# Optimization experiments

Hardware: AMD Instinct MI355X
Metric: run time of the kernel (lower is better)

The kernel has to match this reference:

```python
import jax, jax.numpy as jnp
import numpy as np

B, A, C, L, NH, SCALE = 1, 5, 64, 4, 8, 2
H = W = 24
S = 2 * C
KS = 5


def layernorm(x, g, b, eps=1e-5):
    m = x.mean(-1, keepdims=True)
    v = ((x - m) ** 2).mean(-1, keepdims=True)
    return (x - m) * jax.lax.rsqrt(v + eps) * g + b


def pe_1d(n, d):
    # PositionEncoding: temperature**(2*(i//2)/d), sin of even cols then cos of odd cols
    g = jnp.arange(d, dtype=jnp.float32)
    g = 10000.0 ** (2.0 * jnp.floor(g / 2.0) / d)
    p = jnp.arange(n, dtype=jnp.float32)[:, None] / g[None, :]
    return jnp.concatenate([jnp.sin(p[:, 0::2]), jnp.cos(p[:, 1::2])], axis=1)  # [n, d]


def mha(qk, v, in_w, out_w, nh, mask=None):
    # qk, v: [Lq, Bt, D]; torch nn.MultiheadAttention, bias-free, q=k=qk, value=v
    Lq, Bt, D = qk.shape
    dh = D // nh
    wq, wk, wv = jnp.split(in_w, 3, axis=0)
    q = (qk @ wq.T).reshape(Lq, Bt, nh, dh)
    k = (qk @ wk.T).reshape(Lq, Bt, nh, dh)
    vv = (v @ wv.T).reshape(Lq, Bt, nh, dh)
    s = jnp.einsum('lbhd,mbhd->bhlm', q, k) / jnp.sqrt(jnp.float32(dh))
    if mask is not None:
        s = s + mask
    a = jax.nn.softmax(s, axis=-1)
    o = jnp.einsum('bhlm,mbhd->lbhd', a, vv).reshape(Lq, Bt, D)
    return o @ out_w.T


def unfold3x3(x):
    # F.unfold(k=3, pad=1).permute(2,0,1): [N,c,h,w] -> [h*w, N, 9c] (c, kh, kw ordering)
    N, c, h, w = x.shape
    xp = jnp.pad(x, ((0, 0), (0, 0), (1, 1), (1, 1)))
    p = jnp.stack([xp[:, :, i:i + h, j:j + w] for i in range(3) for j in range(3)], axis=2)
    return p.reshape(N, c * 9, h * w).transpose(2, 0, 1)


def conv_hw(x5, w):
    # Conv3d kernel (1,3,3) pad (0,1,1): 2D conv per angular view
    Bc, Ci, Aa, h, w_ = x5.shape
    y = jax.lax.conv_general_dilated(
        x5.transpose(0, 2, 1, 3, 4).reshape(Bc * Aa, Ci, h, w_), w, (1, 1), ((1, 1), (1, 1)),
        dimension_numbers=('NCHW', 'OIHW', 'NCHW'))
    return y.reshape(Bc, Aa, w.shape[0], h, w_).transpose(0, 2, 1, 3, 4)


def window_mask(h, w, k):
    # SpaTrans.gen_mask: additive -inf outside a k x k local window
    kl, kr = k // 2, k - k // 2
    i = jnp.arange(h)
    j = jnp.arange(w)
    mh = (i[None, :] >= i[:, None] - kl) & (i[None, :] < i[:, None] + kr)
    mw = (j[None, :] >= j[:, None] - kl) & (j[None, :] < j[:, None] + kr)
    m = (mh[:, None, :, None] & mw[None, :, None, :]).reshape(h * w, h * w)
    return jnp.where(m, 0.0, -jnp.inf).astype(jnp.float32)


def setup_inputs() -> dict:
    key = jax.random.key(0)
    ks = iter(jax.random.split(key, 64))
    def nrm(shape, s=0.02):
        return jax.random.normal(next(ks), shape, dtype=jnp.float32) * s
    d = {}
    d['lr'] = jax.random.normal(next(ks), (B, 1, A * H, A * W), dtype=jnp.float32)
    Hh, Wh = H * SCALE, W * SCALE
    ch = -1.0 + (2.0 * jnp.arange(Hh, dtype=jnp.float32) + 1.0) / Hh
    cw = -1.0 + (2.0 * jnp.arange(Wh, dtype=jnp.float32) + 1.0) / Wh
    g = jnp.stack(jnp.meshgrid(ch, cw, indexing='ij'), axis=-1).reshape(-1, 2)
    d['coord'] = jnp.broadcast_to(g, (B, Hh * Wh, 2))
    d['conv0_w'] = nrm((C, 1, 3, 3), 0.1)
    d['convi_w'] = nrm((3, C, C, 3, 3), 0.05)
    d['ang_ln_g'] = jnp.ones((L, C)); d['ang_ln_b'] = jnp.zeros((L, C))
    d['ang_in'] = nrm((L, 3 * C, C)); d['ang_out'] = nrm((L, C, C))
    d['ang_ff_g'] = jnp.ones((L, C)); d['ang_ff_b'] = jnp.zeros((L, C))
    d['ang_w1'] = nrm((L, 2 * C, C)); d['ang_w2'] = nrm((L, C, 2 * C))
    d['spa_mlp'] = nrm((L, S, 9 * C))
    d['spa_ln_g'] = jnp.ones((L, S)); d['spa_ln_b'] = jnp.zeros((L, S))
    d['spa_in'] = nrm((L, 3 * S, S)); d['spa_out'] = nrm((L, S, S))
    d['spa_ff_g'] = jnp.ones((L, S)); d['spa_ff_b'] = jnp.zeros((L, S))
    d['spa_w1'] = nrm((L, 2 * S, S)); d['spa_w2'] = nrm((L, S, 2 * S))
    d['spa_lin'] = nrm((L, C, S))
    IN = A * A * C + 2 + 2 * A * A
    d['imp_w0'] = nrm((320, IN)); d['imp_b0'] = jnp.zeros((320,))
    d['imp_w1'] = nrm((320, 320)); d['imp_b1'] = jnp.zeros((320,))
    d['imp_w2'] = nrm((3 * A * A, 320)); d['imp_b2'] = jnp.zeros((3 * A * A,))
    return d


def reference(lr, coord, conv0_w, convi_w, ang_ln_g, ang_ln_b, ang_in, ang_out,
              ang_ff_g, ang_ff_b, ang_w1, ang_w2, spa_mlp, spa_ln_g, spa_ln_b,
              spa_in, spa_out, spa_ff_g, spa_ff_b, spa_w1, spa_w2, spa_lin,
              imp_w0, imp_b0, imp_w1, imp_b1, imp_w2, imp_b2):
    Bn = lr.shape[0]
    # 'b c (a1 h) (a2 w) -> b c (a1 a2) h w'
    x = lr.reshape(Bn, 1, A, H, A, W).transpose(0, 1, 2, 4, 3, 5).reshape(Bn, 1, A * A, H, W)
    spa_pe_img = ((pe_1d(H, C)[:, None, :] + pe_1d(W, C)[None, :, :]) * 0.5).transpose(2, 0, 1)[None]  # [1,C,h,w]
    ang_pe = pe_1d(A * A, C)[:, None, :]  # [A^2,1,C]
    buf = conv_hw(x, conv0_w)
    t = buf
    for i in range(3):
        t = jax.nn.leaky_relu(conv_hw(t, convi_w[i]), 0.2)
    buf = t + buf
    mask = window_mask(H, W, KS)
    blk = buf
    for l in range(L):
        # ---- AngTrans: tokens [A^2, B*h*w, C]
        tok = blk.transpose(2, 0, 3, 4, 1).reshape(A * A, Bn * H * W, C)
        tn = layernorm(tok + ang_pe, ang_ln_g[l], ang_ln_b[l])
        tok = mha(tn, tok, ang_in[l], ang_out[l], NH) + tok
        ff = layernorm(tok, ang_ff_g[l], ang_ff_b[l])
        tok = jax.nn.relu(ff @ ang_w1[l].T) @ ang_w2[l].T + tok
        blk = tok.reshape(A * A, Bn, H, W, C).transpose(1, 4, 0, 2, 3)
        # ---- SpaTrans: tokens [h*w, B*A^2, 2C] with local-window mask
        xb = blk.transpose(0, 2, 1, 3, 4).reshape(Bn * A * A, C, H, W)
        tok = unfold3x3(xb) @ spa_mlp[l].T
        pe_tok = unfold3x3(spa_pe_img) @ spa_mlp[l].T
        tn = layernorm(tok + pe_tok, spa_ln_g[l], spa_ln_b[l])
        tok = mha(tn, tok, spa_in[l], spa_out[l], NH, mask) + tok
        ff = layernorm(tok, spa_ff_g[l], spa_ff_b[l])
        tok = jax.nn.relu(ff @ spa_w1[l].T) @ spa_w2[l].T + tok
        t5 = tok.reshape(H, W, Bn, A * A, S).transpose(2, 4, 3, 0, 1)  # b s a h w
        blk = jnp.einsum('os,bsahw->boahw', spa_lin[l], t5)  # 1x1x1 Conv3d
    buf = blk + buf
    # 'b c (a1 a2) h w -> b c (a1 h) (a2 w)'
    feat_lr = buf.reshape(Bn, C, A, A, H, W).transpose(0, 1, 2, 4, 3, 5).reshape(Bn, C, A * H, A * W)
    Hh, Wh = H * SCALE, W * SCALE
    # per-view bilinear upsample (align_corners=False)
    v = feat_lr.reshape(Bn, C, A, H, A, W).transpose(0, 2, 4, 1, 3, 5).reshape(Bn * A * A, C, H, W)
    v = jax.image.resize(v, (Bn * A * A, C, Hh, Wh), method='bilinear')
    feat_hr = v.reshape(Bn, A, A, C, Hh, Wh).transpose(0, 4, 5, 1, 2, 3).reshape(Bn, Hh, Wh, A * A * C)
    # nearest grid_sample of LR cell-center coords -> relative coord
    c_ = jnp.clip(coord + 1e-6, -1 + 1e-6, 1 - 1e-6)
    ih = jnp.clip(jnp.round(((c_[..., 0] + 1) * H - 1) / 2), 0, H - 1)
    iw = jnp.clip(jnp.round(((c_[..., 1] + 1) * W - 1) / 2), 0, W - 1)
    qh = -1.0 + (2.0 * ih + 1.0) / H
    qw = -1.0 + (2.0 * iw + 1.0) / W
    rel = jnp.stack([(coord[..., 0] - qh) * H, (coord[..., 1] - qw) * W], axis=-1).reshape(Bn, Hh, Wh, 2)
    au = 0.5 + jnp.arange(A, dtype=jnp.float32)  # make_coord ranges [0,A]
    ca = jnp.stack(jnp.meshgrid(au, au, indexing='ij'), axis=-1).reshape(-1)
    ca = jnp.broadcast_to(ca, (Bn, Hh, Wh, 2 * A * A))
    inp = jnp.concatenate([feat_hr, rel, ca], axis=-1)
    h0 = jax.nn.relu(inp @ imp_w0.T + imp_b0)
    h1 = jax.nn.relu(h0 @ imp_w1.T + imp_b1)
    o = h1 @ imp_w2.T + imp_b2
    # 'b h w (a1 a2 c) -> b c (a1 h) (a2 w)', c=3
    return o.reshape(Bn, Hh, Wh, A, A, 3).transpose(0, 5, 3, 1, 4, 2).reshape(Bn, 3, A * Hh, A * Wh)
```

## Files before the change

kernel.cpp:

```cpp
#include <hip/hip_runtime.h>
#include <math.h>

typedef short  s16x4 __attribute__((ext_vector_type(4)));
typedef short  s16x8 __attribute__((ext_vector_type(8)));
typedef float  f32x4 __attribute__((ext_vector_type(4)));

static const size_t PE25_  = 0;
static const size_t SPAPE_ = 2048;
static const size_t X_     = 38912;
static const size_t CAV_   = 53312;
static const size_t PETOK_ = 54272;
static const size_t W9C_   = 349184;
static const size_t W9S_   = 459776;
static const size_t BUF_   = 754688;
static const size_t BLK_   = 1676288;
static const size_t ATOK_  = 2597888;
static const size_t TNF_   = 3519488;
static const size_t STOK_  = 4441088;
static const size_t STOK2_ = 6284288;
static const size_t QKV_   = 9970688;
static const size_t WS_FLOATS = 15500288;
static const size_t T0_ = QKV_ + 2764800;
static const size_t T1_ = T0_ + 921600;
static const size_t ZP_ = QKV_;
static const size_t H0_ = STOK_;
static const size_t H1_ = STOK2_;

__device__ inline ushort f2bf(float x) {
  unsigned u = __float_as_uint(x);
  u += 0x7fffu + ((u >> 16) & 1u);
  return (ushort)(u >> 16);
}
__device__ inline float bf2f(ushort h) { return __uint_as_float(((unsigned)h) << 16); }

__device__ inline void store_split(char* p, f32x4 v) {
  s16x4 hi, lo;
  #pragma unroll
  for (int e = 0; e < 4; ++e) {
    float x = v[e];
    ushort h = f2bf(x);
    ushort l = f2bf(x - bf2f(h));
    hi[e] = (short)h; lo[e] = (short)l;
  }
  *(s16x4*)p = hi;
  *(s16x4*)(p + 1024) = lo;
}

__device__ inline void scatter_split(char* base, int rr, int c6, float v) {
  ushort hi = f2bf(v);
  ushort lo = f2bf(v - bf2f(hi));
  int ks = c6 >> 5, kh = (c6 >> 4) & 1, k4 = (c6 >> 2) & 3;
  int lane2 = (k4 >> 1)*32 + ((rr & 15) << 1) + (k4 & 1);
  int byt = (((rr >> 4)*2 + ks) << 11) + (kh << 9) + (lane2 << 3) + (c6 & 3)*2;
  *(ushort*)(base + byt) = hi;
  *(ushort*)(base + byt + 1024) = lo;
}

__device__ inline void ld_bf16x16(const ushort* p, float* dst) {
  s16x8 a = *(const s16x8*)p;
  s16x8 b = *(const s16x8*)(p + 8);
  #pragma unroll
  for (int e = 0; e < 8; ++e) { dst[e] = bf2f((ushort)a[e]); dst[8 + e] = bf2f((ushort)b[e]); }
}

__device__ inline void slot_decode(int i, int wave, int lane,
                                   int& row, int& kof, int& wo) {
  int idx = (i << 2) + wave;
  int msub = idx >> 2, ks = (idx >> 1) & 1, kh = idx & 1;
  int rsub = (lane >> 1) & 15;
  int ksub = ((lane >> 5) << 3) + ((lane & 1) << 2);
  row = (msub << 4) + rsub;
  kof = (ks << 5) + (kh << 4) + ksub;
  wo = ((msub * 2 + ks) << 11) + (kh << 9) + (lane << 3);
}

__device__ inline void mfma_step(const char* ldsA, const char* ldsB, int lane,
                                 int wr, int wc, f32x4 acc[2][2]) {
  #pragma unroll
  for (int ks = 0; ks < 2; ++ks) {
    s16x8 ah[2], al[2], bh[2], bl[2];
    #pragma unroll
    for (int i = 0; i < 2; ++i) {
      const char* pa = ldsA + (((wr*2 + i)*2 + ks) << 11) + (lane << 4);
      ah[i] = *(const s16x8*)pa;
      al[i] = *(const s16x8*)(pa + 1024);
      const char* pb = ldsB + (((wc*2 + i)*2 + ks) << 11) + (lane << 4);
      bh[i] = *(const s16x8*)pb;
      bl[i] = *(const s16x8*)(pb + 1024);
    }
    #pragma unroll
    for (int i = 0; i < 2; ++i) {
      #pragma unroll
      for (int j = 0; j < 2; ++j) {
        acc[i][j] = __builtin_amdgcn_mfma_f32_16x16x32_bf16(ah[i], bh[j], acc[i][j], 0, 0, 0);
        acc[i][j] = __builtin_amdgcn_mfma_f32_16x16x32_bf16(ah[i], bl[j], acc[i][j], 0, 0, 0);
        acc[i][j] = __builtin_amdgcn_mfma_f32_16x16x32_bf16(al[i], bh[j], acc[i][j], 0, 0, 0);
      }
    }
  }
}

__device__ inline void epilogue(f32x4 acc[2][2], const float* bias, const float* res,
                                float* out, int N, int m0, int n0,
                                int wr, int wc, int lane, int act) {
  int colb = n0 + wc*32 + (lane & 15);
  int rowb = m0 + wr*32 + ((lane >> 4) << 2);
  #pragma unroll
  for (int j = 0; j < 2; ++j) {
    int cc = colb + j*16;
    if (cc >= N) continue;
    float bv = bias ? bias[cc] : 0.f;
    #pragma unroll
    for (int i = 0; i < 2; ++i) {
      #pragma unroll
      for (int r = 0; r < 4; ++r) {
        int rr = rowb + i*16 + r;
        float v = acc[i][j][r] + bv;
        if (act == 1) v = fmaxf(v, 0.f);
        else if (act == 2) v = v > 0.f ? v : 0.2f*v;
        if (res) v += res[(long)rr*N + cc];
        if (act == 3) {
          int hh = rr / 48, ww2 = rr % 48, q = cc / 3, ch = cc % 3;
          out[ch*57600 + ((q/5)*48 + hh)*240 + (q%5)*48 + ww2] = v;
        } else if (act == 4) {
          ((ushort*)out)[(long)rr*N + cc] = f2bf(v);
        } else {
          out[(long)rr*N + cc] = v;
        }
      }
    }
  }
}

template<int K>
__global__ __launch_bounds__(256) void qkvg_k(
    const float* __restrict__ A, const float* __restrict__ pe, int pe_mode,
    const float* __restrict__ g, const float* __restrict__ bb,
    const float* __restrict__ W, float* __restrict__ out,
    int NTr0, int NTr1, int N, int Mreal, int Mpad) {
  constexpr int NCH = K / 64;
  __shared__ char Apl[NCH * 16384];
  __shared__ char Bp[16384];
  __shared__ float sw_[4][64][2];
  __shared__ float sf_[64][2];
  int bid = blockIdx.x;
  int type = bid / Mpad, m = bid % Mpad;
  if (m >= Mreal) return;
  int m0 = m*64;
  int NTr = type ? NTr1 : NTr0;
  int ntbase = type ? NTr0 : 0;
  int t = threadIdx.x, lane = t & 63, wave = t >> 6;
  int wr = wave >> 1, wc = wave & 1;

  if (type == 0) {
    f32x4 rv[NCH][4];
    float sA[4], sQ[4];
    #pragma unroll
    for (int i = 0; i < 4; ++i) { sA[i] = 0.f; sQ[i] = 0.f; }
    #pragma unroll
    for (int ch = 0; ch < NCH; ++ch)
      #pragma unroll
      for (int i = 0; i < 4; ++i) {
        int row, kof, wo;
        slot_decode(i, wave, lane, row, kof, wo);
        int gk = ch*64 + kof;
        f32x4 av = *(const f32x4*)&A[(long)(m0 + row)*K + gk];
        if (pe_mode == 0)      av += *(const f32x4*)&pe[(long)(m0/576)*K + gk];
        else                   av += *(const f32x4*)&pe[(long)(m0%576 + row)*K + gk];
        rv[ch][i] = av;
        #pragma unroll
        for (int e = 0; e < 4; ++e) { sA[i] += av[e]; sQ[i] = fmaf(av[e], av[e], sQ[i]); }
      }
    #pragma unroll
    for (int i = 0; i < 4; ++i) {
      float s = sA[i], q = sQ[i];
      s += __shfl_xor(s, 1, 64);  q += __shfl_xor(q, 1, 64);
      s += __shfl_xor(s, 32, 64); q += __shfl_xor(q, 32, 64);
      if ((lane & 1) == 0 && lane < 32) {
        int row = i*16 + (lane >> 1);
        sw_[wave][row][0] = s; sw_[wave][row][1] = q;
      }
    }
    __syncthreads();
    if (t < 64) {
      float s = sw_[0][t][0] + sw_[1][t][0] + sw_[2][t][0] + sw_[3][t][0];
      float q = sw_[0][t][1] + sw_[1][t][1] + sw_[2][t][1] + sw_[3][t][1];
      float mean = s / K, var = q / K - mean*mean;
      sf_[t][0] = mean; sf_[t][1] = rsqrtf(var + 1e-5f);
    }
    __syncthreads();
    #pragma unroll
    for (int ch = 0; ch < NCH; ++ch)
      #pragma unroll
      for (int i = 0; i < 4; ++i) {
        int row, kof, wo;
        slot_decode(i, wave, lane, row, kof, wo);
        int gk = ch*64 + kof;
        float mean = sf_[row][0], rstd = sf_[row][1];
        f32x4 gv = *(const f32x4*)&g[gk];
        f32x4 bv = *(const f32x4*)&bb[gk];
        f32x4 nv;
        #pragma unroll
        for (int e = 0; e < 4; ++e) nv[e] = (rv[ch][i][e] - mean)*rstd*gv[e] + bv[e];
        store_split(Apl + ch*16384 + wo, nv);
      }
  } else {
    #pragma unroll
    for (int ch = 0; ch < NCH; ++ch)
      #pragma unroll
      for (int i = 0; i < 4; ++i) {
        int row, kof, wo;
        slot_decode(i, wave, lane, row, kof, wo);
        f32x4 av = *(const f32x4*)&A[(long)(m0 + row)*K + ch*64 + kof];
        store_split(Apl + ch*16384 + wo, av);
      }
  }

  int S = NTr * NCH;
  f32x4 pb[4];
  #pragma unroll
  for (int i = 0; i < 4; ++i) {
    int row, kof, wo;
    slot_decode(i, wave, lane, row, kof, wo);
    pb[i] = *(const f32x4*)&W[(long)(ntbase*64 + row)*K + kof];
  }
  f32x4 acc[2][2];
  #pragma unroll
  for (int i = 0; i < 2; ++i)
    #pragma unroll
    for (int j = 0; j < 2; ++j) acc[i][j] = (f32x4){0.f,0.f,0.f,0.f};
  for (int s = 0; s < S; ++s) {
    int nt = s / NCH, ch = s % NCH;
    __syncthreads();
    #pragma unroll
    for (int i = 0; i < 4; ++i) {
      int row, kof, wo;
      slot_decode(i, wave, lane, row, kof, wo);
      store_split(Bp + wo, pb[i]);
    }
    __syncthreads();
    if (s + 1 < S) {
      int ntn = (s+1) / NCH, chn = (s+1) % NCH;
      #pragma unroll
      for (int i = 0; i < 4; ++i) {
        int row, kof, wo;
        slot_decode(i, wave, lane, row, kof, wo);
        pb[i] = *(const f32x4*)&W[(long)((ntbase+ntn)*64 + row)*K + chn*64 + kof];
      }
    }
    mfma_step(Apl + ch*16384, Bp, lane, wr, wc, acc);
    if (ch == NCH - 1) {
      epilogue(acc, nullptr, nullptr, out, N, m0, (ntbase+nt)*64, wr, wc, lane, 4);
      #pragma unroll
      for (int i = 0; i < 2; ++i)
        #pragma unroll
        for (int j = 0; j < 2; ++j) acc[i][j] = (f32x4){0.f,0.f,0.f,0.f};
    }
  }
}

template<int K, int LN>
__global__ __launch_bounds__(256) void mgemm3_k(
    const float* __restrict__ A, const float* __restrict__ A2, int nsplit,
    const float* __restrict__ pe, int pe_mode,
    const float* __restrict__ g, const float* __restrict__ bb,
    const float* __restrict__ W, const float* __restrict__ bias,
    const float* __restrict__ res, float* __restrict__ out,
    int N, int act, int Mreal, int Mpad) {
  constexpr int NCH = K / 64;
  __shared__ char Apl[NCH * 16384];
  __shared__ char Bp[16384];
  int bid = blockIdx.x;
  int m = bid % Mpad, nt = bid / Mpad;
  if (m >= Mreal) return;
  int m0 = m*64, n0 = nt*64;
  int t = threadIdx.x, lane = t & 63, wave = t >> 6;
  int wr = wave >> 1, wc = wave & 1;
  const float* As = LN ? A2 : A;
  #pragma unroll
  for (int ch = 0; ch < NCH; ++ch)
    #pragma unroll
    for (int i = 0; i < 4; ++i) {
      int row, kof, wo;
      slot_decode(i, wave, lane, row, kof, wo);
      f32x4 av = *(const f32x4*)&As[(long)(m0 + row)*K + ch*64 + kof];
      store_split(Apl + ch*16384 + wo, av);
    }
  f32x4 pb[4];
  #pragma unroll
  for (int i = 0; i < 4; ++i) {
    int row, kof, wo;
    slot_decode(i, wave, lane, row, kof, wo);
    int br = n0 + row;
    pb[i] = (br < N) ? *(const f32x4*)&W[(long)br*K + kof] : (f32x4){0.f,0.f,0.f,0.f};
  }
  __syncthreads();
  f32x4 acc[2][2];
  #pragma unroll
  for (int i = 0; i < 2; ++i)
    #pragma unroll
    for (int j = 0; j < 2; ++j) acc[i][j] = (f32x4){0.f,0.f,0.f,0.f};
  for (int ch = 0; ch < NCH; ++ch) {
    #pragma unroll
    for (int i = 0; i < 4; ++i) {
      int row, kof, wo;
      slot_decode(i, wave, lane, row, kof, wo);
      store_split(Bp + wo, pb[i]);
    }
    __syncthreads();
    if (ch + 1 < NCH) {
      #pragma unroll
      for (int i = 0; i < 4; ++i) {
        int row, kof, wo;
        slot_decode(i, wave, lane, row, kof, wo);
        int br = n0 + row;
        pb[i] = (br < N) ? *(const f32x4*)&W[(long)br*K + (ch+1)*64 + kof]
                         : (f32x4){0.f,0.f,0.f,0.f};
      }
    }
    mfma_step(Apl + ch*16384, Bp, lane, wr, wc, acc);
    if (ch + 1 < NCH) __syncthreads();
  }
  epilogue(acc, bias, res, out, N, m0, n0, wr, wc, lane, act);
}

__global__ __launch_bounds__(256) void cgemm3_k(
    const float* __restrict__ in, const float* __restrict__ W9, long wstride,
    const float* __restrict__ res, float* __restrict__ out, long ostride,
    int N, int act, int Mreal, int Mpad) {
  __shared__ float halo[144 * 68];
  __shared__ char Ap[16384], Bp[16384];
  int bid = blockIdx.x;
  int m = bid % Mpad, nt = bid / Mpad;
  if (m >= Mreal) return;
  int ly = blockIdx.y;
  W9  += (long)ly * wstride;
  out += (long)ly * ostride;
  int m0 = m*64, n0 = nt*64;
  int a = m0 / 576, off = m0 % 576;
  int h_lo = off/24 - 1, h_hi = (off + 63)/24 + 1;
  int RH = h_hi - h_lo + 1;
  int t = threadIdx.x, lane = t & 63, wave = t >> 6;
  int wr = wave >> 1, wc = wave & 1;
  for (int sidx = t; sidx < RH*24*16; sidx += 256) {
    int tokr = sidx >> 4, c4 = (sidx & 15) << 2;
    int h = h_lo + tokr/24, w = tokr % 24;
    f32x4 v = {0.f,0.f,0.f,0.f};
    if ((unsigned)h < 24u) v = *(const f32x4*)&in[(long)(a*576 + h*24 + w)*64 + c4];
    *(f32x4*)&halo[tokr*68 + c4] = v;
  }
  f32x4 pb[4];
  #pragma unroll
  for (int i = 0; i < 4; ++i) {
    int row, kof, wo;
    slot_decode(i, wave, lane, row, kof, wo);
    int br = n0 + row;
    pb[i] = (br < N) ? *(const f32x4*)&W9[(long)br*64 + kof] : (f32x4){0.f,0.f,0.f,0.f};
  }
  __syncthreads();
  f32x4 acc[2][2];
  #pragma unroll
  for (int i = 0; i < 2; ++i)
    #pragma unroll
    for (int j = 0; j < 2; ++j) acc[i][j] = (f32x4){0.f,0.f,0.f,0.f};
  for (int ij = 0; ij < 9; ++ij) {
    int di = ij/3 - 1, dj = ij%3 - 1;
    #pragma unroll
    for (int i = 0; i < 4; ++i) {
      int row, kof, wo;
      slot_decode(i, wave, lane, row, kof, wo);
      int tok = off + row;
      int h2 = tok/24 + di, w2 = tok%24 + dj;
      f32x4 v = {0.f,0.f,0.f,0.f};
      if ((unsigned)h2 < 24u && (unsigned)w2 < 24u)
        v = *(const f32x4*)&halo[((h2 - h_lo)*24 + w2)*68 + kof];
      store_split(Ap + wo, v);
      store_split(Bp + wo, pb[i]);
    }
    __syncthreads();
    if (ij < 8) {
      #pragma unroll
      for (int i = 0; i < 4; ++i) {
        int row, kof, wo;
        slot_decode(i, wave, lane, row, kof, wo);
        int br = n0 + row;
        pb[i] = (br < N) ? *(const f32x4*)&W9[((long)(ij+1)*N + br)*64 + kof]
                         : (f32x4){0.f,0.f,0.f,0.f};
      }
    }
    mfma_step(Ap, Bp, lane, wr, wc, acc);
    if (ij < 8) __syncthreads();
  }
  epilogue(acc, nullptr, res, out, N, m0, n0, wr, wc, lane, act);
}

__global__ __launch_bounds__(256) void ang_mega_k(
    const ushort* __restrict__ qkv, const float* __restrict__ Wout,
    const float* __restrict__ blkr, const float* __restrict__ g,
    const float* __restrict__ bb, float* __restrict__ atok, float* __restrict__ tnf) {
  int hw = blockIdx.x;
  __shared__ float lq[25*192];
  __shared__ float lao[25*64];
  __shared__ float po[25*68];
  __shared__ float wout[64*65];
  __shared__ float st[25][2];
  int t = threadIdx.x;
  for (int idx = t; idx < 600; idx += 256) {
    int a3 = idx / 24, c8 = (idx % 24) * 8;
    s16x8 r = *(const s16x8*)&qkv[(long)(a3*576 + hw)*192 + c8];
    #pragma unroll
    for (int e = 0; e < 8; ++e) lq[a3*192 + c8 + e] = bf2f((ushort)r[e]);
  }
  for (int idx = t; idx < 4096; idx += 256) {
    int c = idx >> 6, d = idx & 63;
    wout[c*65 + d] = Wout[idx];
  }
  __syncthreads();
  if (t < 200) {
    int l = t / 8, head = t & 7;
    const float* q = lq + l*192 + head*8;
    float s[25]; float mx = -1e30f;
    #pragma unroll
    for (int mm = 0; mm < 25; ++mm) {
      const float* kk = lq + mm*192 + 64 + head*8;
      float acc = 0.f;
      #pragma unroll
      for (int d = 0; d < 8; ++d) acc = fmaf(q[d], kk[d], acc);
      acc *= 0.3535533905932738f;
      s[mm] = acc; mx = fmaxf(mx, acc);
    }
    float sum = 0.f;
    #pragma unroll
    for (int mm = 0; mm < 25; ++mm) { s[mm] = expf(s[mm] - mx); sum += s[mm]; }
    float inv = 1.f / sum;
    #pragma unroll
    for (int d = 0; d < 8; ++d) {
      float acc = 0.f;
      #pragma unroll
      for (int mm = 0; mm < 25; ++mm) acc = fmaf(s[mm], lq[mm*192 + 128 + head*8 + d], acc);
      lao[l*64 + head*8 + d] = acc * inv;
    }
  }
  __syncthreads();
  for (int idx = t; idx < 1600; idx += 256) {
    int tok = idx >> 6, c = idx & 63;
    const float* ar = &lao[tok*64];
    const float* wr = &wout[c*65];
    float accp = 0.f;
    #pragma unroll 16
    for (int d = 0; d < 64; ++d) accp = fmaf(ar[d], wr[d], accp);
    po[tok*68 + c] = accp + blkr[(long)(tok*576 + hw)*64 + c];
  }
  __syncthreads();
  if (t < 25) {
    float s = 0.f, q = 0.f;
    for (int c = 0; c < 64; ++c) { float x = po[t*68 + c]; s += x; q = fmaf(x, x, q); }
    float mean = s / 64.f, var = q / 64.f - mean*mean;
    st[t][0] = mean; st[t][1] = rsqrtf(var + 1e-5f);
  }
  __syncthreads();
  for (int idx = t; idx < 1600; idx += 256) {
    int tok = idx >> 6, c = idx & 63;
    float x = po[tok*68 + c];
    long gidx = (long)(tok*576 + hw)*64 + c;
    atok[gidx] = x;
    tnf[gidx] = (x - st[tok][0]) * st[tok][1] * g[c] + bb[c];
  }
}

__global__ __launch_bounds__(256) void ffn_ang_k(
    const float* __restrict__ tnf, const float* __restrict__ w1,
    const float* __restrict__ w2, float* __restrict__ atok,
    int Mreal, int Mpad) {
  __shared__ char Ap[16384], Bp[16384], Hp[2][16384];
  int bid = blockIdx.x;
  int m = bid % Mpad;
  if (m >= Mreal) return;
  int m0 = m*64;
  int t = threadIdx.x, lane = t & 63, wave = t >> 6;
  int wr = wave >> 1, wc = wave & 1;
  #pragma unroll
  for (int i = 0; i < 4; ++i) {
    int row, kof, wo;
    slot_decode(i, wave, lane, row, kof, wo);
    f32x4 av = *(const f32x4*)&tnf[(long)(m0 + row)*64 + kof];
    store_split(Ap + wo, av);
  }
  f32x4 pb[4];
  #pragma unroll
  for (int i = 0; i < 4; ++i) {
    int row, kof, wo;
    slot_decode(i, wave, lane, row, kof, wo);
    pb[i] = *(const f32x4*)&w1[(long)row*64 + kof];
  }
  __syncthreads();
  for (int nt = 0; nt < 2; ++nt) {
    #pragma unroll
    for (int i = 0; i < 4; ++i) {
      int row, kof, wo;
      slot_decode(i, wave, lane, row, kof, wo);
      store_split(Bp + wo, pb[i]);
    }
    __syncthreads();
    #pragma unroll
    for (int i = 0; i < 4; ++i) {
      int row, kof, wo;
      slot_decode(i, wave, lane, row, kof, wo);
      pb[i] = (nt == 0) ? *(const f32x4*)&w1[(long)(64 + row)*64 + kof]
                        : *(const f32x4*)&w2[(long)row*128 + kof];
    }
    f32x4 acc[2][2];
    #pragma unroll
    for (int i = 0; i < 2; ++i)
      #pragma unroll
      for (int j = 0; j < 2; ++j) acc[i][j] = (f32x4){0.f,0.f,0.f,0.f};
    mfma_step(Ap, Bp, lane, wr, wc, acc);
    #pragma unroll
    for (int jj = 0; jj < 2; ++jj)
      #pragma unroll
      for (int ii = 0; ii < 2; ++ii)
        #pragma unroll
        for (int r = 0; r < 4; ++r) {
          int rr = wr*32 + ii*16 + ((lane >> 4) << 2) + r;
          int cc = wc*32 + jj*16 + (lane & 15);
          scatter_split(Hp[nt], rr, cc, fmaxf(acc[ii][jj][r], 0.f));
        }
    __syncthreads();
  }
  f32x4 acc2[2][2];
  #pragma unroll
  for (int i = 0; i < 2; ++i)
    #pragma unroll
    for (int j = 0; j < 2; ++j) acc2[i][j] = (f32x4){0.f,0.f,0.f,0.f};
  for (int ch = 0; ch < 2; ++ch) {
    #pragma unroll
    for (int i = 0; i < 4; ++i) {
      int row, kof, wo;
      slot_decode(i, wave, lane, row, kof, wo);
      store_split(Bp + wo, pb[i]);
    }
    __syncthreads();
    if (ch == 0) {
      #pragma unroll
      for (int i = 0; i < 4; ++i) {
        int row, kof, wo;
        slot_decode(i, wave, lane, row, kof, wo);
        pb[i] = *(const f32x4*)&w2[(long)row*128 + 64 + kof];
      }
    }
    mfma_step(Hp[ch], Bp, lane, wr, wc, acc2);
    if (ch == 0) __syncthreads();
  }
  epilogue(acc2, nullptr, atok, atok, 64, m0, 0, wr, wc, lane, 0);
}

__global__ __launch_bounds__(512) void megaspa_k(
    const ushort* __restrict__ qkv, const float* __restrict__ stok,
    const float* __restrict__ wout, const float* __restrict__ g,
    const float* __restrict__ bb, const float* __restrict__ w1,
    const float* __restrict__ w2, const float* __restrict__ wlin,
    float* __restrict__ outb, int Mreal, int Mpad) {
  __shared__ char Aop[32768];
  __shared__ char SCR[65536];
  __shared__ float Rf[64*132];
  __shared__ float st[64][2];
  int bid = blockIdx.x;
  int m = bid % Mpad;
  if (m >= Mreal) return;
  int m0 = m*64;
  int t = threadIdx.x, lane = t & 63, wave = t >> 6;
  int wgrp = wave >> 2, w4 = wave & 3;
  int wr = w4 >> 1, wc = w4 & 1;
  char* Bp  = SCR + wgrp*16384;
  char* Hp0 = SCR + 32768;
  char* Hp1 = SCR + 49152;

  for (int idx = t; idx < 2048; idx += 512) {
    int row = idx >> 5, c4 = (idx & 31) << 2;
    *(f32x4*)&Rf[row*132 + c4] = *(const f32x4*)&stok[(long)(m0 + row)*128 + c4];
  }
  f32x4 pw[2][4];
  #pragma unroll
  for (int ch = 0; ch < 2; ++ch)
    #pragma unroll
    for (int i = 0; i < 4; ++i) {
      int row, kof, wo;
      slot_decode(i, w4, lane, row, kof, wo);
      pw[ch][i] = *(const f32x4*)&wout[(long)(wgrp*64 + row)*128 + ch*64 + kof];
    }

  {
    int rr1 = t >> 3, head = t & 7;
    int x = m0 + rr1;
    int hw = x % 576, h = hw / 24, w = hw % 24;
    float qr[16];
    ld_bf16x16(qkv + (long)x*384 + head*16, qr);
    float s[25]; float mx = -1e30f;
    #pragma unroll
    for (int ro = 0; ro < 5; ++ro) {
      int h2 = h + ro - 2;
      s16x8 k0[5], k1[5];
      #pragma unroll
      for (int co = 0; co < 5; ++co) {
        int xt = x + (ro - 2)*24 + (co - 2);
        xt = min(max(xt, 0), 14399);
        const ushort* kp = qkv + (long)xt*384 + 128 + head*16;
        k0[co] = *(const s16x8*)kp;
        k1[co] = *(const s16x8*)(kp + 8);
      }
      #pragma unroll
      for (int co = 0; co < 5; ++co) {
        int w2c = w + co - 2;
        float sc = -1e30f;
        if (h2 >= 0 && h2 < 24 && w2c >= 0 && w2c < 24) {
          sc = 0.f;
          #pragma unroll
          for (int d = 0; d < 8; ++d) sc = fmaf(qr[d], bf2f((ushort)k0[co][d]), sc);
          #pragma unroll
          for (int d = 0; d < 8; ++d) sc = fmaf(qr[8+d], bf2f((ushort)k1[co][d]), sc);
          sc *= 0.25f;
        }
        s[ro*5 + co] = sc; mx = fmaxf(mx, sc);
      }
    }
    float sum = 0.f;
    #pragma unroll
    for (int i = 0; i < 25; ++i) {
      float e = (s[i] > -1e29f) ? expf(s[i] - mx) : 0.f;
      s[i] = e; sum += e;
    }
    float inv = 1.f / sum;
    float acc[16];
    #pragma unroll
    for (int d = 0; d < 16; ++d) acc[d] = 0.f;
    #pragma unroll
    for (int ro = 0; ro < 5; ++ro) {
      s16x8 v0[5], v1[5];
      #pragma unroll
      for (int co = 0; co < 5; ++co) {
        int xt = x + (ro - 2)*24 + (co - 2);
        xt = min(max(xt, 0), 14399);
        const ushort* vp = qkv + (long)xt*384 + 256 + head*16;
        v0[co] = *(const s16x8*)vp;
        v1[co] = *(const s16x8*)(vp + 8);
      }
      #pragma unroll
      for (int co = 0; co < 5; ++co) {
        float sv = s[ro*5 + co];
        #pragma unroll
        for (int d = 0; d < 8; ++d) acc[d] = fmaf(sv, bf2f((ushort)v0[co][d]), acc[d]);
        #pragma unroll
        for (int d = 0; d < 8; ++d) acc[8+d] = fmaf(sv, bf2f((ushort)v1[co][d]), acc[8+d]);
      }
    }
    #pragma unroll
    for (int d = 0; d < 16; ++d) {
      int cc = head*16 + d;
      scatter_split(Aop + (cc >> 6)*16384, rr1, cc & 63, acc[d] * inv);
    }
  }

  {
    int nt = wgrp;
    f32x4 acc[2][2];
    #pragma unroll
    for (int i = 0; i < 2; ++i)
      #pragma unroll
      for (int j = 0; j < 2; ++j) acc[i][j] = (f32x4){0.f,0.f,0.f,0.f};
    for (int ch = 0; ch < 2; ++ch) {
      __syncthreads();
      #pragma unroll
      for (int i = 0; i < 4; ++i) {
        int row, kof, wo;
        slot_decode(i, w4, lane, row, kof, wo);
        store_split(Bp + wo, pw[ch][i]);
      }
      __syncthreads();
      mfma_step(Aop + ch*16384, Bp, lane, wr, wc, acc);
    }
    int colb = nt*64 + wc*32 + (lane & 15);
    int rowb = wr*32 + ((lane >> 4) << 2);
    #pragma unroll
    for (int j = 0; j < 2; ++j)
      #pragma unroll
      for (int i = 0; i < 2; ++i)
        #pragma unroll
        for (int r = 0; r < 4; ++r) {
          int rr = rowb + i*16 + r, cc = colb + j*16;
          Rf[rr*132 + cc] += acc[i][j][r];
        }
  }
  __syncthreads();

  {
    int row = t >> 3, q8 = t & 7;
    const float* yr = &Rf[row*132 + q8*16];
    float sm = 0.f, sq = 0.f;
    #pragma unroll
    for (int j2 = 0; j2 < 16; ++j2) { float xv = yr[j2]; sm += xv; sq = fmaf(xv, xv, sq); }
    sm += __shfl_xor(sm, 1, 64); sq += __shfl_xor(sq, 1, 64);
    sm += __shfl_xor(sm, 2, 64); sq += __shfl_xor(sq, 2, 64);
    sm += __shfl_xor(sm, 4, 64); sq += __shfl_xor(sq, 4, 64);
    if (q8 == 0) {
      float mean = sm / 128.f, var = sq / 128.f - mean*mean;
      st[row][0] = mean; st[row][1] = rsqrtf(var + 1e-5f);
    }
  }
  __syncthreads();
  {
    int ch = wgrp;
    #pragma unroll
    for (int i = 0; i < 4; ++i) {
      int row, kof, wo;
      slot_decode(i, w4, lane, row, kof, wo);
      int gk = ch*64 + kof;
      f32x4 xv = *(const f32x4*)&Rf[row*132 + gk];
      float mean = st[row][0], rstd = st[row][1];
      f32x4 gv = *(const f32x4*)&g[gk];
      f32x4 bv = *(const f32x4*)&bb[gk];
      f32x4 nv;
      #pragma unroll
      for (int e = 0; e < 4; ++e) nv[e] = (xv[e] - mean)*rstd*gv[e] + bv[e];
      store_split(Aop + ch*16384 + wo, nv);
    }
  }

  f32x4 acc2[2][2];
  #pragma unroll
  for (int i = 0; i < 2; ++i)
    #pragma unroll
    for (int j = 0; j < 2; ++j) acc2[i][j] = (f32x4){0.f,0.f,0.f,0.f};
  for (int r = 0; r < 2; ++r) {
    int nt = 2*r + wgrp;
    f32x4 accH[2][2];
    #pragma unroll
    for (int i = 0; i < 2; ++i)
      #pragma unroll
      for (int j = 0; j < 2; ++j) accH[i][j] = (f32x4){0.f,0.f,0.f,0.f};
    for (int ch = 0; ch < 2; ++ch) {
      __syncthreads();
      #pragma unroll
      for (int i = 0; i < 4; ++i) {
        int row, kof, wo;
        slot_decode(i, w4, lane, row, kof, wo);
        f32x4 bv = *(const f32x4*)&w1[(long)(nt*64 + row)*128 + ch*64 + kof];
        store_split(Bp + wo, bv);
      }
      __syncthreads();
      mfma_step(Aop + ch*16384, Bp, lane, wr, wc, accH);
    }
    char* Hpw = wgrp ? Hp1 : Hp0;
    #pragma unroll
    for (int jj = 0; jj < 2; ++jj)
      #pragma unroll
      for (int ii = 0; ii < 2; ++ii)
        #pragma unroll
        for (int rx = 0; rx < 4; ++rx) {
          int rr = wr*32 + ii*16 + ((lane >> 4) << 2) + rx;
          int cc = wc*32 + jj*16 + (lane & 15);
          scatter_split(Hpw, rr, cc, fmaxf(accH[ii][jj][rx], 0.f));
        }
    for (int q = 0; q < 2; ++q) {
      __syncthreads();
      #pragma unroll
      for (int i = 0; i < 4; ++i) {
        int row, kof, wo;
        slot_decode(i, w4, lane, row, kof, wo);
        f32x4 bv = *(const f32x4*)&w2[(long)(wgrp*64 + row)*256 + (2*r + q)*64 + kof];
        store_split(Bp + wo, bv);
      }
      __syncthreads();
      mfma_step(q ? Hp1 : Hp0, Bp, lane, wr, wc, acc2);
    }
  }
  {
    int colb = wc*32 + (lane & 15);
    int rowb = wr*32 + ((lane >> 4) << 2);
    #pragma unroll
    for (int jj = 0; jj < 2; ++jj)
      #pragma unroll
      for (int ii = 0; ii < 2; ++ii)
        #pragma unroll
        for (int rx = 0; rx < 4; ++rx) {
          int rr = rowb + ii*16 + rx;
          int cc = colb + jj*16;
          scatter_split(Aop + wgrp*16384, rr, cc,
                        acc2[ii][jj][rx] + Rf[rr*132 + wgrp*64 + cc]);
        }
  }

  f32x4 acc3[2][2];
  #pragma unroll
  for (int i = 0; i < 2; ++i)
    #pragma unroll
    for (int j = 0; j < 2; ++j) acc3[i][j] = (f32x4){0.f,0.f,0.f,0.f};
  for (int ch = 0; ch < 2; ++ch) {
    __syncthreads();
    if (wgrp == 0) {
      #pragma unroll
      for (int i = 0; i < 4; ++i) {
        int row, kof, wo;
        slot_decode(i, w4, lane, row, kof, wo);
        f32x4 bv = *(const f32x4*)&wlin[(long)row*128 + ch*64 + kof];
        store_split(SCR + wo, bv);
      }
    }
    __syncthreads();
    if (wgrp == 0) mfma_step(Aop + ch*16384, SCR, lane, wr, wc, acc3);
  }
  if (wgrp == 0)
    epilogue(acc3, nullptr, nullptr, outb, 64, m0, 0, wr, wc, lane, 0);
}

__global__ __launch_bounds__(256) void zgemm3_k(
    const float* __restrict__ buf, const float* __restrict__ blk,
    const float* __restrict__ W0, float* __restrict__ Zp) {
  __shared__ char Ap[16384], Bp[16384];
  int bid = blockIdx.x;
  int m = bid % 9;
  int nz = bid / 9;
  int n = nz % 5, z = nz / 5;
  int m0 = m*64, n0 = n*64;
  int t = threadIdx.x, lane = t & 63, wave = t >> 6;
  int wr = wave >> 1, wc = wave & 1;
  f32x4 pa[4], pb[4];
  #pragma unroll
  for (int i = 0; i < 4; ++i) {
    int row, kof, wo;
    slot_decode(i, wave, lane, row, kof, wo);
    long tok = (long)(z*5)*576 + m0 + row;
    pa[i] = *(const f32x4*)&buf[tok*64 + kof];
    pa[i] += *(const f32x4*)&blk[tok*64 + kof];
    pb[i] = *(const f32x4*)&W0[(long)(n0 + row)*1652 + (z*5)*64 + kof];
  }
  f32x4 acc[2][2];
  #pragma unroll
  for (int i = 0; i < 2; ++i)
    #pragma unroll
    for (int j = 0; j < 2; ++j) acc[i][j] = (f32x4){0.f,0.f,0.f,0.f};
  for (int q = 0; q < 5; ++q) {
    #pragma unroll
    for (int i = 0; i < 4; ++i) {
      int row, kof, wo;
      slot_decode(i, wave, lane, row, kof, wo);
      store_split(Ap + wo, pa[i]);
      store_split(Bp + wo, pb[i]);
    }
    __syncthreads();
    if (q < 4) {
      #pragma unroll
      for (int i = 0; i < 4; ++i) {
        int row, kof, wo;
        slot_decode(i, wave, lane, row, kof, wo);
        long tok = (long)(z*5 + q + 1)*576 + m0 + row;
        pa[i] = *(const f32x4*)&buf[tok*64 + kof];
        pa[i] += *(const f32x4*)&blk[tok*64 + kof];
        pb[i] = *(const f32x4*)&W0[(long)(n0 + row)*1652 + (z*5 + q + 1)*64 + kof];
      }
    }
    mfma_step(Ap, Bp, lane, wr, wc, acc);
    if (q < 4) __syncthreads();
  }
  epilogue(acc, nullptr, nullptr, Zp + (long)z*184320, 320, m0, n0, wr, wc, lane, 0);
}

__global__ void combine_k(const float* __restrict__ Zp, const float* __restrict__ cav,
                          const float* __restrict__ coord, float* __restrict__ h0out) {
  int gidx = blockIdx.x * 256 + threadIdx.x;
  if (gidx >= 2304 * 320) return;
  int p = gidx / 320, o = gidx % 320;
  int hh = p / 48, ww = p % 48;
  float sh = hh * 0.5f - 0.25f, sw = ww * 0.5f - 0.25f;
  int h0i = (int)floorf(sh); float fh = sh - h0i;
  int w0i = (int)floorf(sw); float fw = sw - w0i;
  int h0c = max(h0i, 0), h1c = min(h0i + 1, 23);
  int w0c = max(w0i, 0), w1c = min(w0i + 1, 23);
  int i00 = (h0c*24 + w0c)*320 + o, i01 = (h0c*24 + w1c)*320 + o;
  int i10 = (h1c*24 + w0c)*320 + o, i11 = (h1c*24 + w1c)*320 + o;
  float z00 = 0.f, z01 = 0.f, z10 = 0.f, z11 = 0.f;
  #pragma unroll
  for (int z = 0; z < 5; ++z) {
    const float* Zz = Zp + (long)z*184320;
    z00 += Zz[i00]; z01 += Zz[i01]; z10 += Zz[i10]; z11 += Zz[i11];
  }
  float v = (1.f-fh)*((1.f-fw)*z00 + fw*z01) + fh*((1.f-fw)*z10 + fw*z11);
  #pragma unroll
  for (int d = 0; d < 2; ++d) {
    float co = coord[p*2 + d];
    float cc = fminf(fmaxf(co + 1e-6f, -1.f + 1e-6f), 1.f - 1e-6f);
    float ix = rintf(((cc + 1.f)*24.f - 1.f)*0.5f);
    ix = fminf(fmaxf(ix, 0.f), 23.f);
    float q = -1.f + (2.f*ix + 1.f)/24.f;
    v = fmaf((co - q)*24.f, cav[320*(d+1) + o], v);
  }
  h0out[gidx] = fmaxf(v + cav[o], 0.f);
}

__device__ inline float pe_val(int pos, int c) {
  int j = c & 31;
  float freq = powf(10000.f, -2.f * (float)j / 64.f);
  float arg = (float)pos * freq;
  return (c < 32) ? sinf(arg) : cosf(arg);
}

__global__ void setup_k(const float* __restrict__ lr, const float* __restrict__ convi_w,
                        const float* __restrict__ spa_mlp,
                        const float* __restrict__ imp_w0, const float* __restrict__ imp_b0,
                        float* pe25, float* spa_pe, float* X, float* w9c, float* w9s,
                        float* cav) {
  int g = blockIdx.x * 256 + threadIdx.x;
  if (g < 1600) { pe25[g] = pe_val(g >> 6, g & 63); return; }
  g -= 1600;
  if (g < 36864) {
    int hw = g >> 6, c = g & 63; int h = hw / 24, w = hw % 24;
    spa_pe[g] = 0.5f * (pe_val(h, c) + pe_val(w, c)); return;
  }
  g -= 36864;
  if (g < 14400) {
    int aa = g / 576, hw = g % 576, h = hw / 24, w = hw % 24;
    X[g] = lr[((aa/5)*24 + h)*120 + (aa%5)*24 + w]; return;
  }
  g -= 14400;
  if (g < 110592) {
    int cv = g / 36864, rem = g % 36864;
    int ij = rem / 4096, oc = rem % 4096;
    int o = oc >> 6, c = oc & 63;
    w9c[g] = convi_w[((long)(cv*64 + o)*64 + c)*9 + ij]; return;
  }
  g -= 110592;
  if (g < 294912) {
    int l = g / 73728, rem = g % 73728;
    int ij = rem / 8192, oc = rem % 8192;
    int o = oc >> 6, c = oc & 63;
    w9s[g] = spa_mlp[((long)(l*128 + o))*576 + c*9 + ij]; return;
  }
  g -= 294912;
  if (g < 320) {
    int o = g;
    float s = imp_b0[o];
    #pragma unroll
    for (int idx = 0; idx < 50; ++idx) {
      int pair = idx >> 1;
      float cvv = 0.5f + (float)((idx & 1) ? pair % 5 : pair / 5);
      s = fmaf(cvv, imp_w0[(long)o*1652 + 1602 + idx], s);
    }
    cav[o] = s;
    cav[320 + o] = imp_w0[(long)o*1652 + 1600];
    cav[640 + o] = imp_w0[(long)o*1652 + 1601];
  }
}

__global__ void conv0_k(const float* __restrict__ X, const float* __restrict__ W,
                        float* __restrict__ out) {
  int sp = threadIdx.x >> 6, lane = threadIdx.x & 63;
  int strip = blockIdx.x * 4 + sp;
  int a = strip / 48, r = strip % 48, h = r >> 1, w0 = (r & 1) * 12;
  __shared__ float patch[4][3][16];
  if (lane < 42) {
    int i = lane / 14, col = lane % 14;
    int h2 = h + i - 1, w2 = w0 + col - 1;
    float v = 0.f;
    if ((unsigned)h2 < 24u && (unsigned)w2 < 24u) v = X[a*576 + h2*24 + w2];
    patch[sp][i][col] = v;
  }
  __syncthreads();
  float wv[9];
  #pragma unroll
  for (int q = 0; q < 9; ++q) wv[q] = W[lane*9 + q];
  #pragma unroll
  for (int p = 0; p < 12; ++p) {
    float acc = 0.f;
    #pragma unroll
    for (int i = 0; i < 3; ++i)
      #pragma unroll
      for (int j = 0; j < 3; ++j)
        acc = fmaf(patch[sp][i][p + j], wv[i*3 + j], acc);
    out[(long)(a*576 + h*24 + w0 + p)*64 + lane] = acc;
  }
}

extern "C" void kernel_launch(void* const* d_in, const int* in_sizes, int n_in,
                              void* d_out, int out_size, void* d_ws, size_t ws_size,
                              hipStream_t stream) {
  (void)in_sizes; (void)n_in; (void)out_size;
  if (ws_size < (size_t)WS_FLOATS * 4) return;
  float* ws = (float*)d_ws;

  const float* lr       = (const float*)d_in[0];
  const float* coord    = (const float*)d_in[1];
  const float* conv0_w  = (const float*)d_in[2];
  const float* convi_w  = (const float*)d_in[3];
  const float* ang_ln_g = (const float*)d_in[4];
  const float* ang_ln_b = (const float*)d_in[5];
  const float* ang_in   = (const float*)d_in[6];
  const float* ang_out  = (const float*)d_in[7];
  const float* ang_ff_g = (const float*)d_in[8];
  const float* ang_ff_b = (const float*)d_in[9];
  const float* ang_w1   = (const float*)d_in[10];
  const float* ang_w2   = (const float*)d_in[11];
  const float* spa_mlp  = (const float*)d_in[12];
  const float* spa_ln_g = (const float*)d_in[13];
  const float* spa_ln_b = (const float*)d_in[14];
  const float* spa_in   = (const float*)d_in[15];
  const float* spa_out  = (const float*)d_in[16];
  const float* spa_ff_g = (const float*)d_in[17];
  const float* spa_ff_b = (const float*)d_in[18];
  const float* spa_w1   = (const float*)d_in[19];
  const float* spa_w2   = (const float*)d_in[20];
  const float* spa_lin  = (const float*)d_in[21];
  const float* imp_w0   = (const float*)d_in[22];
  const float* imp_b0   = (const float*)d_in[23];
  const float* imp_w1   = (const float*)d_in[24];
  const float* imp_b1   = (const float*)d_in[25];
  const float* imp_w2   = (const float*)d_in[26];
  const float* imp_b2   = (const float*)d_in[27];

  float* pe25 = ws + PE25_;  float* spa_pe = ws + SPAPE_;  float* X = ws + X_;
  float* cav = ws + CAV_;    float* petok = ws + PETOK_;
  float* w9c = ws + W9C_;    float* w9s = ws + W9S_;
  float* buf = ws + BUF_;    float* blk = ws + BLK_;      float* atok = ws + ATOK_;
  float* tnf = ws + TNF_;    float* stok = ws + STOK_;
  float* qkvf = ws + QKV_;   ushort* qkvh = (ushort*)(ws + QKV_);
  float* t0 = ws + T0_;      float* t1 = ws + T1_;
  float* Zp = ws + ZP_;      float* h0 = ws + H0_;        float* h1 = ws + H1_;

  setup_k<<<1792, 256, 0, stream>>>(lr, convi_w, spa_mlp, imp_w0, imp_b0,
                                    pe25, spa_pe, X, w9c, w9s, cav);
  conv0_k<<<300, 256, 0, stream>>>(X, conv0_w, buf);
  cgemm3_k<<<dim3(232,1), 256, 0, stream>>>(buf, w9c,         0, nullptr, t0,  0, 64, 2, 225, 232);
  cgemm3_k<<<dim3(232,1), 256, 0, stream>>>(t0,  w9c + 36864, 0, nullptr, t1,  0, 64, 2, 225, 232);
  cgemm3_k<<<dim3(232,1), 256, 0, stream>>>(t1,  w9c + 73728, 0, buf,     buf, 0, 64, 2, 225, 232);
  cgemm3_k<<<dim3(32, 4), 256, 0, stream>>>(spa_pe, w9s, 73728, nullptr, petok, 73728,
                                            128, 0, 9, 16);

  for (int l = 0; l < 4; ++l) {
    const float* blkr = (l == 0) ? buf : blk;
    qkvg_k<64><<<464, 256, 0, stream>>>(blkr, pe25, 0,
        ang_ln_g + l*64, ang_ln_b + l*64, ang_in + l*192*64, qkvf,
        2, 1, 192, 225, 232);
    ang_mega_k<<<576, 256, 0, stream>>>(qkvh, ang_out + l*64*64, blkr,
        ang_ff_g + l*64, ang_ff_b + l*64, atok, tnf);
    ffn_ang_k<<<232, 256, 0, stream>>>(tnf, ang_w1 + l*128*64, ang_w2 + l*64*128,
        atok, 225, 232);
    cgemm3_k<<<dim3(464,1), 256, 0, stream>>>(atok, w9s + l*73728, 0, nullptr, stok, 0,
        128, 0, 225, 232);
    qkvg_k<128><<<464, 256, 0, stream>>>(stok, petok + l*73728, 1,
        spa_ln_g + l*128, spa_ln_b + l*128, spa_in + l*384*128, qkvf,
        4, 2, 384, 225, 232);
    megaspa_k<<<232, 512, 0, stream>>>(qkvh, stok, spa_out + l*128*128,
        spa_ff_g + l*128, spa_ff_b + l*128, spa_w1 + l*256*128, spa_w2 + l*128*256,
        spa_lin + l*64*128, blk, 225, 232);
  }

  zgemm3_k<<<225, 256, 0, stream>>>(buf, blk, imp_w0, Zp);
  combine_k<<<2880, 256, 0, stream>>>(Zp, cav, coord, h0);
  mgemm3_k<320,0><<<200, 256, 0, stream>>>(h0, h0, 0, nullptr, -1, nullptr, nullptr,
      imp_w1, imp_b1, nullptr, h1, 320, 1, 36, 40);
  mgemm3_k<320,0><<<80, 256, 0, stream>>>(h1, h1, 0, nullptr, -1, nullptr, nullptr,
      imp_w2, imp_b2, nullptr, (float*)d_out, 75, 3, 36, 40);
}
```

Measured before the change: 553.8 us.

## Loop output-column tiles inside conv GEMM and batch weight staging in megaspa

The 3x3 conv GEMM kernel now processes all N tiles for one M tile inside a single block. The halo load is reused across N tiles, and the grid is half the size for N=128 convs. In megaspa, the out-projection and linear weight tiles are staged into separate shared scratch regions with one barrier instead of per-chunk barriers. ang_mega_k's Wout load is vectorised. The trade-off is fewer blocks (less parallelism) and more serial work per block.

```diff
diff --git a/kernel.cpp b/kernel.cpp
--- a/kernel.cpp
+++ b/kernel.cpp
@@ -327,16 +327,16 @@
 __global__ __launch_bounds__(256) void cgemm3_k(
     const float* __restrict__ in, const float* __restrict__ W9, long wstride,
     const float* __restrict__ res, float* __restrict__ out, long ostride,
-    int N, int act, int Mreal, int Mpad) {
+    int N, int NTr, int act, int Mreal, int Mpad) {
   __shared__ float halo[144 * 68];
   __shared__ char Ap[16384], Bp[16384];
   int bid = blockIdx.x;
-  int m = bid % Mpad, nt = bid / Mpad;
+  int m = bid % Mpad;
   if (m >= Mreal) return;
   int ly = blockIdx.y;
   W9  += (long)ly * wstride;
   out += (long)ly * ostride;
-  int m0 = m*64, n0 = nt*64;
+  int m0 = m*64;
   int a = m0 / 576, off = m0 % 576;
   int h_lo = off/24 - 1, h_hi = (off + 63)/24 + 1;
   int RH = h_hi - h_lo + 1;
@@ -354,16 +354,17 @@
   for (int i = 0; i < 4; ++i) {
     int row, kof, wo;
     slot_decode(i, wave, lane, row, kof, wo);
-    int br = n0 + row;
-    pb[i] = (br < N) ? *(const f32x4*)&W9[(long)br*64 + kof] : (f32x4){0.f,0.f,0.f,0.f};
-  }
-  __syncthreads();
+    pb[i] = (row < N) ? *(const f32x4*)&W9[(long)row*64 + kof] : (f32x4){0.f,0.f,0.f,0.f};
+  }
+  __syncthreads();
+  int S = NTr * 9;
   f32x4 acc[2][2];
   #pragma unroll
   for (int i = 0; i < 2; ++i)
     #pragma unroll
     for (int j = 0; j < 2; ++j) acc[i][j] = (f32x4){0.f,0.f,0.f,0.f};
-  for (int ij = 0; ij < 9; ++ij) {
+  for (int s = 0; s < S; ++s) {
+    int nt = s / 9, ij = s % 9;
     int di = ij/3 - 1, dj = ij%3 - 1;
     #pragma unroll
     for (int i = 0; i < 4; ++i) {
@@ -378,20 +379,27 @@
       store_split(Bp + wo, pb[i]);
     }
     __syncthreads();
-    if (ij < 8) {
+    if (s + 1 < S) {
+      int ntn = (s+1) / 9, ijn = (s+1) % 9;
       #pragma unroll
       for (int i = 0; i < 4; ++i) {
         int row, kof, wo;
         slot_decode(i, wave, lane, row, kof, wo);
-        int br = n0 + row;
-        pb[i] = (br < N) ? *(const f32x4*)&W9[((long)(ij+1)*N + br)*64 + kof]
+        int br = ntn*64 + row;
+        pb[i] = (br < N) ? *(const f32x4*)&W9[((long)ijn*N + br)*64 + kof]
                          : (f32x4){0.f,0.f,0.f,0.f};
       }
     }
     mfma_step(Ap, Bp, lane, wr, wc, acc);
-    if (ij < 8) __syncthreads();
-  }
-  epilogue(acc, nullptr, res, out, N, m0, n0, wr, wc, lane, act);
+    if (ij == 8) {
+      epilogue(acc, nullptr, res, out, N, m0, nt*64, wr, wc, lane, act);
+      #pragma unroll
+      for (int i = 0; i < 2; ++i)
+        #pragma unroll
+        for (int j = 0; j < 2; ++j) acc[i][j] = (f32x4){0.f,0.f,0.f,0.f};
+    }
+    if (s + 1 < S) __syncthreads();
+  }
 }
 
 __global__ __launch_bounds__(256) void ang_mega_k(
@@ -411,9 +419,11 @@
     #pragma unroll
     for (int e = 0; e < 8; ++e) lq[a3*192 + c8 + e] = bf2f((ushort)r[e]);
   }
-  for (int idx = t; idx < 4096; idx += 256) {
-    int c = idx >> 6, d = idx & 63;
-    wout[c*65 + d] = Wout[idx];
+  for (int idx = t; idx < 1024; idx += 256) {
+    f32x4 wv = *(const f32x4*)&Wout[idx*4];
+    int c = (idx*4) >> 6, d = (idx*4) & 63;
+    #pragma unroll
+    for (int e = 0; e < 4; ++e) wout[c*65 + d + e] = wv[e];
   }
   __syncthreads();
   if (t < 200) {
@@ -661,23 +671,23 @@
   }
 
   {
-    int nt = wgrp;
-    f32x4 acc[2][2];
-    #pragma unroll
-    for (int i = 0; i < 2; ++i)
-      #pragma unroll
-      for (int j = 0; j < 2; ++j) acc[i][j] = (f32x4){0.f,0.f,0.f,0.f};
-    for (int ch = 0; ch < 2; ++ch) {
-      __syncthreads();
+    #pragma unroll
+    for (int ch = 0; ch < 2; ++ch)
       #pragma unroll
       for (int i = 0; i < 4; ++i) {
         int row, kof, wo;
         slot_decode(i, w4, lane, row, kof, wo);
-        store_split(Bp + wo, pw[ch][i]);
-      }
-      __syncthreads();
-      mfma_step(Aop + ch*16384, Bp, lane, wr, wc, acc);
-    }
+        store_split(SCR + (wgrp*2 + ch)*16384 + wo, pw[ch][i]);
+      }
+    __syncthreads();
+    int nt = wgrp;
+    f32x4 acc[2][2];
+    #pragma unroll
+    for (int i = 0; i < 2; ++i)
+      #pragma unroll
+      for (int j = 0; j < 2; ++j) acc[i][j] = (f32x4){0.f,0.f,0.f,0.f};
+    for (int ch = 0; ch < 2; ++ch)
+      mfma_step(Aop + ch*16384, SCR + (wgrp*2 + ch)*16384, lane, wr, wc, acc);
     int colb = nt*64 + wc*32 + (lane & 15);
     int rowb = wr*32 + ((lane >> 4) << 2);
     #pragma unroll
@@ -789,27 +799,28 @@
         }
   }
 
-  f32x4 acc3[2][2];
-  #pragma unroll
-  for (int i = 0; i < 2; ++i)
-    #pragma unroll
-    for (int j = 0; j < 2; ++j) acc3[i][j] = (f32x4){0.f,0.f,0.f,0.f};
-  for (int ch = 0; ch < 2; ++ch) {
-    __syncthreads();
-    if (wgrp == 0) {
-      #pragma unroll
-      for (int i = 0; i < 4; ++i) {
-        int row, kof, wo;
-        slot_decode(i, w4, lane, row, kof, wo);
-        f32x4 bv = *(const f32x4*)&wlin[(long)row*128 + ch*64 + kof];
-        store_split(SCR + wo, bv);
-      }
-    }
-    __syncthreads();
-    if (wgrp == 0) mfma_step(Aop + ch*16384, SCR, lane, wr, wc, acc3);
-  }
-  if (wgrp == 0)
+  __syncthreads();
+  {
+    int ch = wgrp;
+    #pragma unroll
+    for (int i = 0; i < 4; ++i) {
+      int row, kof, wo;
+      slot_decode(i, w4, lane, row, kof, wo);
+      f32x4 bv = *(const f32x4*)&wlin[(long)row*128 + ch*64 + kof];
+      store_split(SCR + ch*16384 + wo, bv);
+    }
+  }
+  __syncthreads();
+  if (wgrp == 0) {
+    f32x4 acc3[2][2];
+    #pragma unroll
+    for (int i = 0; i < 2; ++i)
+      #pragma unroll
+      for (int j = 0; j < 2; ++j) acc3[i][j] = (f32x4){0.f,0.f,0.f,0.f};
+    for (int ch = 0; ch < 2; ++ch)
+      mfma_step(Aop + ch*16384, SCR + ch*16384, lane, wr, wc, acc3);
     epilogue(acc3, nullptr, nullptr, outb, 64, m0, 0, wr, wc, lane, 0);
+  }
 }
 
 __global__ __launch_bounds__(256) void zgemm3_k(
@@ -1027,11 +1038,11 @@
   setup_k<<<1792, 256, 0, stream>>>(lr, convi_w, spa_mlp, imp_w0, imp_b0,
                                     pe25, spa_pe, X, w9c, w9s, cav);
   conv0_k<<<300, 256, 0, stream>>>(X, conv0_w, buf);
-  cgemm3_k<<<dim3(232,1), 256, 0, stream>>>(buf, w9c,         0, nullptr, t0,  0, 64, 2, 225, 232);
-  cgemm3_k<<<dim3(232,1), 256, 0, stream>>>(t0,  w9c + 36864, 0, nullptr, t1,  0, 64, 2, 225, 232);
-  cgemm3_k<<<dim3(232,1), 256, 0, stream>>>(t1,  w9c + 73728, 0, buf,     buf, 0, 64, 2, 225, 232);
-  cgemm3_k<<<dim3(32, 4), 256, 0, stream>>>(spa_pe, w9s, 73728, nullptr, petok, 73728,
-                                            128, 0, 9, 16);
+  cgemm3_k<<<dim3(232,1), 256, 0, stream>>>(buf, w9c,         0, nullptr, t0,  0, 64, 1, 2, 225, 232);
+  cgemm3_k<<<dim3(232,1), 256, 0, stream>>>(t0,  w9c + 36864, 0, nullptr, t1,  0, 64, 1, 2, 225, 232);
+  cgemm3_k<<<dim3(232,1), 256, 0, stream>>>(t1,  w9c + 73728, 0, buf,     buf, 0, 64, 1, 2, 225, 232);
+  cgemm3_k<<<dim3(16, 4), 256, 0, stream>>>(spa_pe, w9s, 73728, nullptr, petok, 73728,
+                                            128, 2, 0, 9, 16);
 
   for (int l = 0; l < 4; ++l) {
     const float* blkr = (l == 0) ? buf : blk;
@@ -1042,8 +1053,8 @@
         ang_ff_g + l*64, ang_ff_b + l*64, atok, tnf);
     ffn_ang_k<<<232, 256, 0, stream>>>(tnf, ang_w1 + l*128*64, ang_w2 + l*64*128,
         atok, 225, 232);
-    cgemm3_k<<<dim3(464,1), 256, 0, stream>>>(atok, w9s + l*73728, 0, nullptr, stok, 0,
-        128, 0, 225, 232);
+    cgemm3_k<<<dim3(232,1), 256, 0, stream>>>(atok, w9s + l*73728, 0, nullptr, stok, 0,
+        128, 2, 0, 225, 232);
     qkvg_k<128><<<464, 256, 0, stream>>>(stok, petok + l*73728, 1,
         spa_ln_g + l*128, spa_ln_b + l*128, spa_in + l*384*128, qkvf,
         4, 2, 384, 225, 232);
```

Result: slower. 632.9 us (+14.3%).
